# Kernel optimization log

Measured on AMD Instinct MI355X. Metric: run time of the kernel, lower is better.

## Reference

```python
import jax, jax.numpy as jnp
import numpy as np

N_NODES = 4096
IN_FEAT = 256
N_HEADS = 8
N_HIDDEN = 64  # out_features // n_heads
NEG_SLOPE = 0.2
EDGE_PROB = 0.05


def setup_inputs() -> dict:
    key = jax.random.key(0)
    k1, k2, k3, k4 = jax.random.split(key, 4)
    h = jax.random.normal(k1, (N_NODES, IN_FEAT), dtype=jnp.float32)
    # binary adjacency mask [N, N, 1] (broadcast over heads), as in the torch asserts
    adj_mat = (jax.random.uniform(k2, (N_NODES, N_NODES, 1)) < EDGE_PROB).astype(jnp.float32)
    # nn.Linear(in_features, n_heads*n_hidden, bias=False) weight: [H*F, in]
    W = jax.random.normal(k3, (N_HEADS * N_HIDDEN, IN_FEAT), dtype=jnp.float32) / np.sqrt(IN_FEAT)
    # nn.Linear(2*n_hidden, 1, bias=False) weight, flattened: [2*F]
    a = jax.random.normal(k4, (2 * N_HIDDEN,), dtype=jnp.float32) / np.sqrt(2 * N_HIDDEN)
    return {"h": h, "adj_mat": adj_mat, "W": W, "a": a}


def reference(h, adj_mat, W, a):
    n = h.shape[0]
    # g: [N, H, F]
    g = (h @ W.T).reshape(n, N_HEADS, N_HIDDEN)
    # attn(cat[g_i, g_j]) == a_l . g_i + a_r . g_j  (linear, no bias)
    a_l = a[:N_HIDDEN]
    a_r = a[N_HIDDEN:]
    el = jnp.einsum('ihf,f->ih', g, a_l)  # [N, H]
    er = jnp.einsum('jhf,f->jh', g, a_r)  # [N, H]
    e = jax.nn.leaky_relu(el[:, None, :] + er[None, :, :], NEG_SLOPE)  # [N, N, H]
    # note: original multiplies scores by adjacency (not masked_fill)
    e = e * adj_mat  # adj broadcasts over heads
    att = jax.nn.softmax(e, axis=1)  # softmax over source nodes j
    # dropout is identity at eval (dropout_rate=0.0)
    out = jnp.einsum('ijh,jhf->ihf', att, g)  # [N, H, F]
    return out.reshape(n, N_HEADS * N_HIDDEN)
```

## Files before the change

### kernel.cpp

```cpp
#include <hip/hip_runtime.h>

#define N_NODES 4096
#define IN_FEAT 256
#define N_HEADS 8
#define N_HIDDEN 64
#define OUT_FEAT (N_HEADS * N_HIDDEN)
#define NEG_SLOPE 0.2f

typedef _Float16 half8 __attribute__((ext_vector_type(8)));
typedef _Float16 h2 __attribute__((ext_vector_type(2)));
typedef float floatx4 __attribute__((ext_vector_type(4)));

__global__ __launch_bounds__(256) void produce(
    const float* __restrict__ H, const float* __restrict__ adj,
    const float* __restrict__ Wt, const float* __restrict__ a,
    _Float16* __restrict__ GT16, float* __restrict__ elT,
    _Float16* __restrict__ eR1h, _Float16* __restrict__ eR2h,
    unsigned long long* __restrict__ bits) {
  __shared__ _Float16 SM[4 * 64 * 64];
  const int t = threadIdx.x;
  const int bx = blockIdx.x, by = blockIdx.y;

  if (by >= 8) {
    const int c = bx * 8 + (by - 8);
    const size_t W0 = (size_t)c * 512;
    const int wv = t >> 6, lane = t & 63;
    for (int k0 = 0; k0 < 128; k0 += 8) {
      float v[8];
#pragma unroll
      for (int k = 0; k < 8; ++k)
        v[k] = adj[(W0 + wv * 128 + k0 + k) * 64 + lane];
#pragma unroll
      for (int k = 0; k < 8; ++k) {
        unsigned long long m = __ballot(v[k] != 0.f);
        if (lane == 0) bits[W0 + wv * 128 + k0 + k] = m;
      }
    }
    return;
  }

  _Float16* Ah = SM;
  _Float16* Al = SM + 4096;
  _Float16* Bh = SM + 8192;
  _Float16* Bl = SM + 12288;
  const int w = t >> 6, l = t & 63;
  const int n16 = l & 15, q = l >> 4;
  const int bi = bx, bo = by;
  const int m0 = bi * 64 + w * 16;

  floatx4 acc[4];
#pragma unroll
  for (int ct = 0; ct < 4; ++ct) acc[ct] = (floatx4)0.f;

  for (int kc = 0; kc < 4; ++kc) {
    if (kc) __syncthreads();
#pragma unroll
    for (int p = 0; p < 4; ++p) {
      const int idx = p * 256 + t;
      const int r = idx >> 4;
      const int c4 = (idx & 15) << 2;
      const int dst = r * 64 + ((((idx & 15) >> 1)) ^ (r & 7)) * 8 + (idx & 1) * 4;
      float4 hv = *(const float4*)(H + (size_t)(bi * 64 + r) * IN_FEAT + kc * 64 + c4);
      float4 wv = *(const float4*)(Wt + (size_t)(bo * 64 + r) * IN_FEAT + kc * 64 + c4);
      union { _Float16 h[4]; int2 d; } hh_, hl_, wh_, wl_;
      hh_.h[0] = (_Float16)hv.x; hh_.h[1] = (_Float16)hv.y;
      hh_.h[2] = (_Float16)hv.z; hh_.h[3] = (_Float16)hv.w;
      hl_.h[0] = (_Float16)(hv.x - (float)hh_.h[0]);
      hl_.h[1] = (_Float16)(hv.y - (float)hh_.h[1]);
      hl_.h[2] = (_Float16)(hv.z - (float)hh_.h[2]);
      hl_.h[3] = (_Float16)(hv.w - (float)hh_.h[3]);
      wh_.h[0] = (_Float16)wv.x; wh_.h[1] = (_Float16)wv.y;
      wh_.h[2] = (_Float16)wv.z; wh_.h[3] = (_Float16)wv.w;
      wl_.h[0] = (_Float16)(wv.x - (float)wh_.h[0]);
      wl_.h[1] = (_Float16)(wv.y - (float)wh_.h[1]);
      wl_.h[2] = (_Float16)(wv.z - (float)wh_.h[2]);
      wl_.h[3] = (_Float16)(wv.w - (float)wh_.h[3]);
      *(int2*)&Ah[dst] = hh_.d;
      *(int2*)&Al[dst] = hl_.d;
      *(int2*)&Bh[dst] = wh_.d;
      *(int2*)&Bl[dst] = wl_.d;
    }
    __syncthreads();
#pragma unroll
    for (int ks = 0; ks < 2; ++ks) {
      const int ao = (w * 16 + n16) * 64 + (((ks << 2) + q) ^ (n16 & 7)) * 8;
      half8 Afh = *(const half8*)&Ah[ao];
      half8 Afl = *(const half8*)&Al[ao];
#pragma unroll
      for (int ct = 0; ct < 4; ++ct) {
        const int bofs = (ct * 16 + n16) * 64 + (((ks << 2) + q) ^ (n16 & 7)) * 8;
        half8 Bfh = *(const half8*)&Bh[bofs];
        half8 Bfl = *(const half8*)&Bl[bofs];
        acc[ct] = __builtin_amdgcn_mfma_f32_16x16x32_f16(Afh, Bfh, acc[ct], 0, 0, 0);
        acc[ct] = __builtin_amdgcn_mfma_f32_16x16x32_f16(Afl, Bfh, acc[ct], 0, 0, 0);
        acc[ct] = __builtin_amdgcn_mfma_f32_16x16x32_f16(Afh, Bfl, acc[ct], 0, 0, 0);
      }
    }
  }

  float aLv[4], aRv[4];
#pragma unroll
  for (int ct = 0; ct < 4; ++ct) {
    aLv[ct] = a[ct * 16 + n16];
    aRv[ct] = a[64 + ct * 16 + n16];
  }
#pragma unroll
  for (int reg = 0; reg < 4; ++reg) {
    float sl = 0.f, sr = 0.f;
#pragma unroll
    for (int ct = 0; ct < 4; ++ct) {
      sl = fmaf(acc[ct][reg], aLv[ct], sl);
      sr = fmaf(acc[ct][reg], aRv[ct], sr);
    }
#pragma unroll
    for (int off = 1; off < 16; off <<= 1) {
      sl += __shfl_xor(sl, off);
      sr += __shfl_xor(sr, off);
    }
    if (n16 == 0) {
      const int rowi = m0 + q * 4 + reg;
      elT[(size_t)bo * N_NODES + rowi] = sl;
      eR1h[(size_t)bo * N_NODES + rowi] = (_Float16)__expf(sr);
      eR2h[(size_t)bo * N_NODES + rowi] = (_Float16)__expf(0.2f * sr);
    }
  }

  __syncthreads();
  _Float16* LG = SM;
#pragma unroll
  for (int ct = 0; ct < 4; ++ct)
#pragma unroll
    for (int reg = 0; reg < 4; ++reg)
      LG[(w * 16 + q * 4 + reg) * 72 + ct * 16 + n16] = (_Float16)acc[ct][reg];
  __syncthreads();
  {
    const int f = t >> 2, jq = t & 3;
    union { _Float16 hh[16]; int4 v[2]; } u;
#pragma unroll
    for (int k = 0; k < 16; ++k) u.hh[k] = LG[(jq * 16 + k) * 72 + f];
    _Float16* dst = GT16 + (size_t)(bo * 64 + f) * N_NODES + bi * 64 + jq * 16;
    *(int4*)dst = u.v[0];
    *(int4*)(dst + 8) = u.v[1];
  }
}

__global__ __launch_bounds__(256) void attn_v6(
    const unsigned long long* __restrict__ bits, const _Float16* __restrict__ GT16,
    const float* __restrict__ elT, const _Float16* __restrict__ eR1h,
    const _Float16* __restrict__ eR2h, float* __restrict__ out) {
  __shared__ __align__(16) _Float16 Gt[2][2][4096];
  __shared__ __align__(16) _Float16 eRs1[2][2][64];
  __shared__ __align__(16) _Float16 eRs2[2][2][64];
  __shared__ uint2 bitsS[2][2][32];
  __shared__ float eL1s[32], eL2s[32];
  __shared__ float Zh1[32], Zfull[32];

  const int t = threadIdx.x;
  const int ib = blockIdx.x, h = blockIdx.y;
  const int i0 = ib * 32;
  const int w = t >> 6, l = t & 63, n16 = l & 15, q = l >> 4;
  const int rt = w & 1, jh = w >> 1;

  const int gjh = t >> 7, sf = (t >> 1) & 63, hrow = t & 1;
  const _Float16* gsrc = GT16 + (size_t)(h * 64 + sf) * N_NODES + gjh * 2048 + hrow * 32;
  const int era = (t >> 3) & 1, erjh = t >> 4, erseg = t & 7;
  const int bro = (t - 32) & 31, brjh = (t - 32) >> 5;

  if (t < 32) {
    float e = elT[(size_t)h * N_NODES + i0 + t];
    eL1s[t] = __expf(e);
    eL2s[t] = __expf(0.2f * e);
  }
  {
#pragma unroll
    for (int g = 0; g < 4; ++g) {
      int4 v = *(const int4*)(gsrc + g * 8);
      *(int4*)&Gt[0][gjh][sf * 64 + ((hrow * 4 + g) ^ (sf & 7)) * 8] = v;
    }
    if (t < 32) {
      const _Float16* esrc = (era ? eR2h : eR1h) + (size_t)h * N_NODES + erjh * 2048 + erseg * 8;
      int4 v = *(const int4*)esrc;
      *(int4*)&(era ? eRs2 : eRs1)[0][erjh][erseg * 8] = v;
    } else if (t < 96) {
      bitsS[0][brjh][bro] = *(const uint2*)&bits[(size_t)(i0 + bro) * 64 + brjh * 32];
    }
  }
  __syncthreads();

  const _Float16 e1f = (_Float16)eL1s[rt * 16 + n16];
  const _Float16 e2f = (_Float16)eL2s[rt * 16 + n16];
  const h2 eL1h2 = {e1f, e1f};
  const h2 eL2h2 = {e2f, e2f};
  half8 Bones;
#pragma unroll
  for (int k = 0; k < 8; ++k) Bones[k] = (n16 == 0) ? (_Float16)1.f : (_Float16)0.f;

  floatx4 acc[4];
#pragma unroll
  for (int ft = 0; ft < 4; ++ft) acc[ft] = (floatx4)0.f;
  floatx4 acc5 = (floatx4)0.f;

  int par = 0;
  for (int step = 0; step < 32; ++step) {
    int4 gv[4]; int4 ev; uint2 bv2;
    const bool more = (step + 1 < 32);
    if (more) {
      const _Float16* gs = gsrc + (size_t)(step + 1) * 64;
#pragma unroll
      for (int g = 0; g < 4; ++g) gv[g] = *(const int4*)(gs + g * 8);
      if (t < 32) {
        const _Float16* esrc = (era ? eR2h : eR1h) + (size_t)h * N_NODES + erjh * 2048 +
                               (step + 1) * 64 + erseg * 8;
        ev = *(const int4*)esrc;
      } else if (t < 96) {
        bv2 = *(const uint2*)&bits[(size_t)(i0 + bro) * 64 + brjh * 32 + step + 1];
      }
    }
    const uint2 bw = bitsS[par][jh][rt * 16 + n16];
    const _Float16* gt = &Gt[par][jh][0];
#pragma unroll
    for (int ks = 0; ks < 2; ++ks) {
      const unsigned dw = ks ? bw.y : bw.x;
      const unsigned byte = (dw >> (q * 8)) & 0xffu;
      uint4 r1 = *(const uint4*)&eRs1[par][jh][ks * 32 + q * 8];
      uint4 r2 = *(const uint4*)&eRs2[par][jh][ks * 32 + q * 8];
      const unsigned r1a[4] = {r1.x, r1.y, r1.z, r1.w};
      const unsigned r2a[4] = {r2.x, r2.y, r2.z, r2.w};
      unsigned pr[4];
#pragma unroll
      for (int kk = 0; kk < 4; ++kk) {
        h2 pa = eL1h2 * __builtin_bit_cast(h2, r1a[kk]);
        h2 pb = eL2h2 * __builtin_bit_cast(h2, r2a[kk]);
        h2 pv = __builtin_elementwise_max(pa, pb);
        unsigned y = (byte >> (2 * kk)) & 3u;
        unsigned b01 = (y | (y << 15)) & 0x00010001u;
        unsigned keep = b01 * 0xffffu;
        pr[kk] = (__builtin_bit_cast(unsigned, pv) & keep) | (0x3C003C00u & ~keep);
      }
      const uint4 prv = {pr[0], pr[1], pr[2], pr[3]};
      half8 Af = __builtin_bit_cast(half8, prv);
#pragma unroll
      for (int ft = 0; ft < 4; ++ft) {
        half8 Bf = *(const half8*)&gt[(ft * 16 + n16) * 64 + (((ks << 2) + q) ^ (n16 & 7)) * 8];
        acc[ft] = __builtin_amdgcn_mfma_f32_16x16x32_f16(Af, Bf, acc[ft], 0, 0, 0);
      }
      acc5 = __builtin_amdgcn_mfma_f32_16x16x32_f16(Af, Bones, acc5, 0, 0, 0);
    }
    if (more) {
      const int np = par ^ 1;
#pragma unroll
      for (int g = 0; g < 4; ++g)
        *(int4*)&Gt[np][gjh][sf * 64 + ((hrow * 4 + g) ^ (sf & 7)) * 8] = gv[g];
      if (t < 32) {
        *(int4*)&(era ? eRs2 : eRs1)[np][erjh][erseg * 8] = ev;
      } else if (t < 96) {
        bitsS[np][brjh][bro] = bv2;
      }
    }
    __syncthreads();
    par ^= 1;
  }

  float* comb = (float*)&Gt[0][0][0];
  if (jh == 1) {
#pragma unroll
    for (int ft = 0; ft < 4; ++ft)
#pragma unroll
      for (int reg = 0; reg < 4; ++reg)
        comb[(rt * 16 + q * 4 + reg) * 68 + ft * 16 + n16] = acc[ft][reg];
    if (n16 == 0) {
#pragma unroll
      for (int reg = 0; reg < 4; ++reg) Zh1[rt * 16 + q * 4 + reg] = acc5[reg];
    }
  }
  __syncthreads();
  if (jh == 0) {
#pragma unroll
    for (int ft = 0; ft < 4; ++ft)
#pragma unroll
      for (int reg = 0; reg < 4; ++reg)
        acc[ft][reg] += comb[(rt * 16 + q * 4 + reg) * 68 + ft * 16 + n16];
    if (n16 == 0) {
#pragma unroll
      for (int reg = 0; reg < 4; ++reg) {
        const int row = rt * 16 + q * 4 + reg;
        Zfull[row] = acc5[reg] + Zh1[row];
      }
    }
  }
  __syncthreads();
  if (jh == 0) {
#pragma unroll
    for (int reg = 0; reg < 4; ++reg) {
      const int row = rt * 16 + q * 4 + reg;
      const float invz = 1.f / Zfull[row];
      float* op = out + (size_t)(i0 + row) * OUT_FEAT + h * 64;
#pragma unroll
      for (int ft = 0; ft < 4; ++ft) op[ft * 16 + n16] = acc[ft][reg] * invz;
    }
  }
}

extern "C" void kernel_launch(void* const* d_in, const int* in_sizes, int n_in,
                              void* d_out, int out_size, void* d_ws, size_t ws_size,
                              hipStream_t stream) {
  const float* h   = (const float*)d_in[0];
  const float* adj = (const float*)d_in[1];
  const float* W   = (const float*)d_in[2];
  const float* a   = (const float*)d_in[3];
  float* out = (float*)d_out;

  char* ws = (char*)d_ws;
  _Float16* GT16 = (_Float16*)ws;
  unsigned long long* bits = (unsigned long long*)(ws + 4u * 1024 * 1024);
  float* elT = (float*)(ws + 6u * 1024 * 1024);
  _Float16* eR1h = (_Float16*)(ws + 6u * 1024 * 1024 + 128 * 1024);
  _Float16* eR2h = (_Float16*)(ws + 6u * 1024 * 1024 + 192 * 1024);

  produce<<<dim3(64, 16), 256, 0, stream>>>(h, adj, W, a, GT16, elT, eR1h, eR2h, bits);
  attn_v6<<<dim3(128, 8), 256, 0, stream>>>(bits, GT16, elT, eR1h, eR2h, out);
}
```

Before: 160.6 us.

## Load MFMA operands directly from global into registers, dropping LDS staging

The attention kernel no longer stages G tiles, eR vectors and adjacency bits through double-buffered shared memory with a barrier every step. Each lane now loads its own MFMA B fragments, eR values and bitmask word straight from global memory into registers, prefetched one step ahead. The launch bound also requests 4 blocks per CU. This removes the LDS round-trip and per-step __syncthreads, but raises register pressure and relies on L1/L2 to absorb the duplicated global reads across waves and blocks.

Measured after the change: 258.7 us. +61.1%, slower.

```diff
diff --git a/kernel.cpp b/kernel.cpp
--- a/kernel.cpp
+++ b/kernel.cpp
@@ -144,14 +144,11 @@
   }
 }
 
-__global__ __launch_bounds__(256) void attn_v6(
+__global__ __launch_bounds__(256, 4) void attn_v7(
     const unsigned long long* __restrict__ bits, const _Float16* __restrict__ GT16,
     const float* __restrict__ elT, const _Float16* __restrict__ eR1h,
     const _Float16* __restrict__ eR2h, float* __restrict__ out) {
-  __shared__ __align__(16) _Float16 Gt[2][2][4096];
-  __shared__ __align__(16) _Float16 eRs1[2][2][64];
-  __shared__ __align__(16) _Float16 eRs2[2][2][64];
-  __shared__ uint2 bitsS[2][2][32];
+  __shared__ float comb[32 * 68];
   __shared__ float eL1s[32], eL2s[32];
   __shared__ float Zh1[32], Zfull[32];
 
@@ -161,29 +158,10 @@
   const int w = t >> 6, l = t & 63, n16 = l & 15, q = l >> 4;
   const int rt = w & 1, jh = w >> 1;
 
-  const int gjh = t >> 7, sf = (t >> 1) & 63, hrow = t & 1;
-  const _Float16* gsrc = GT16 + (size_t)(h * 64 + sf) * N_NODES + gjh * 2048 + hrow * 32;
-  const int era = (t >> 3) & 1, erjh = t >> 4, erseg = t & 7;
-  const int bro = (t - 32) & 31, brjh = (t - 32) >> 5;
-
   if (t < 32) {
     float e = elT[(size_t)h * N_NODES + i0 + t];
     eL1s[t] = __expf(e);
     eL2s[t] = __expf(0.2f * e);
-  }
-  {
-#pragma unroll
-    for (int g = 0; g < 4; ++g) {
-      int4 v = *(const int4*)(gsrc + g * 8);
-      *(int4*)&Gt[0][gjh][sf * 64 + ((hrow * 4 + g) ^ (sf & 7)) * 8] = v;
-    }
-    if (t < 32) {
-      const _Float16* esrc = (era ? eR2h : eR1h) + (size_t)h * N_NODES + erjh * 2048 + erseg * 8;
-      int4 v = *(const int4*)esrc;
-      *(int4*)&(era ? eRs2 : eRs1)[0][erjh][erseg * 8] = v;
-    } else if (t < 96) {
-      bitsS[0][brjh][bro] = *(const uint2*)&bits[(size_t)(i0 + bro) * 64 + brjh * 32];
-    }
   }
   __syncthreads();
 
@@ -195,37 +173,51 @@
 #pragma unroll
   for (int k = 0; k < 8; ++k) Bones[k] = (n16 == 0) ? (_Float16)1.f : (_Float16)0.f;
 
+  const _Float16* gb = GT16 + (size_t)(h * 64 + n16) * N_NODES + jh * 2048 + q * 8;
+  const _Float16* e1p = eR1h + (size_t)h * N_NODES + jh * 2048 + q * 8;
+  const _Float16* e2p = eR2h + (size_t)h * N_NODES + jh * 2048 + q * 8;
+  const unsigned long long* bp = bits + (size_t)(i0 + rt * 16 + n16) * 64 + jh * 32;
+
   floatx4 acc[4];
 #pragma unroll
   for (int ft = 0; ft < 4; ++ft) acc[ft] = (floatx4)0.f;
   floatx4 acc5 = (floatx4)0.f;
 
-  int par = 0;
+  half8 Bc[2][4];
+  uint4 r1c[2], r2c[2];
+  unsigned long long bvc;
+#pragma unroll
+  for (int ks = 0; ks < 2; ++ks) {
+#pragma unroll
+    for (int ft = 0; ft < 4; ++ft)
+      Bc[ks][ft] = *(const half8*)(gb + (size_t)ft * (16 * N_NODES) + ks * 32);
+    r1c[ks] = *(const uint4*)(e1p + ks * 32);
+    r2c[ks] = *(const uint4*)(e2p + ks * 32);
+  }
+  bvc = bp[0];
+
   for (int step = 0; step < 32; ++step) {
-    int4 gv[4]; int4 ev; uint2 bv2;
-    const bool more = (step + 1 < 32);
-    if (more) {
-      const _Float16* gs = gsrc + (size_t)(step + 1) * 64;
-#pragma unroll
-      for (int g = 0; g < 4; ++g) gv[g] = *(const int4*)(gs + g * 8);
-      if (t < 32) {
-        const _Float16* esrc = (era ? eR2h : eR1h) + (size_t)h * N_NODES + erjh * 2048 +
-                               (step + 1) * 64 + erseg * 8;
-        ev = *(const int4*)esrc;
-      } else if (t < 96) {
-        bv2 = *(const uint2*)&bits[(size_t)(i0 + bro) * 64 + brjh * 32 + step + 1];
-      }
-    }
-    const uint2 bw = bitsS[par][jh][rt * 16 + n16];
-    const _Float16* gt = &Gt[par][jh][0];
+    half8 Bn[2][4];
+    uint4 r1n[2], r2n[2];
+    unsigned long long bvn = bvc;
+    if (step + 1 < 32) {
+      const _Float16* gs = gb + (step + 1) * 64;
+#pragma unroll
+      for (int ks = 0; ks < 2; ++ks) {
+#pragma unroll
+        for (int ft = 0; ft < 4; ++ft)
+          Bn[ks][ft] = *(const half8*)(gs + (size_t)ft * (16 * N_NODES) + ks * 32);
+        r1n[ks] = *(const uint4*)(e1p + (step + 1) * 64 + ks * 32);
+        r2n[ks] = *(const uint4*)(e2p + (step + 1) * 64 + ks * 32);
+      }
+      bvn = bp[step + 1];
+    }
 #pragma unroll
     for (int ks = 0; ks < 2; ++ks) {
-      const unsigned dw = ks ? bw.y : bw.x;
+      const unsigned dw = (unsigned)(bvc >> (ks * 32));
       const unsigned byte = (dw >> (q * 8)) & 0xffu;
-      uint4 r1 = *(const uint4*)&eRs1[par][jh][ks * 32 + q * 8];
-      uint4 r2 = *(const uint4*)&eRs2[par][jh][ks * 32 + q * 8];
-      const unsigned r1a[4] = {r1.x, r1.y, r1.z, r1.w};
-      const unsigned r2a[4] = {r2.x, r2.y, r2.z, r2.w};
+      const unsigned r1a[4] = {r1c[ks].x, r1c[ks].y, r1c[ks].z, r1c[ks].w};
+      const unsigned r2a[4] = {r2c[ks].x, r2c[ks].y, r2c[ks].z, r2c[ks].w};
       unsigned pr[4];
 #pragma unroll
       for (int kk = 0; kk < 4; ++kk) {
@@ -240,28 +232,20 @@
       const uint4 prv = {pr[0], pr[1], pr[2], pr[3]};
       half8 Af = __builtin_bit_cast(half8, prv);
 #pragma unroll
-      for (int ft = 0; ft < 4; ++ft) {
-        half8 Bf = *(const half8*)&gt[(ft * 16 + n16) * 64 + (((ks << 2) + q) ^ (n16 & 7)) * 8];
-        acc[ft] = __builtin_amdgcn_mfma_f32_16x16x32_f16(Af, Bf, acc[ft], 0, 0, 0);
-      }
+      for (int ft = 0; ft < 4; ++ft)
+        acc[ft] = __builtin_amdgcn_mfma_f32_16x16x32_f16(Af, Bc[ks][ft], acc[ft], 0, 0, 0);
       acc5 = __builtin_amdgcn_mfma_f32_16x16x32_f16(Af, Bones, acc5, 0, 0, 0);
     }
-    if (more) {
-      const int np = par ^ 1;
-#pragma unroll
-      for (int g = 0; g < 4; ++g)
-        *(int4*)&Gt[np][gjh][sf * 64 + ((hrow * 4 + g) ^ (sf & 7)) * 8] = gv[g];
-      if (t < 32) {
-        *(int4*)&(era ? eRs2 : eRs1)[np][erjh][erseg * 8] = ev;
-      } else if (t < 96) {
-        bitsS[np][brjh][bro] = bv2;
-      }
-    }
-    __syncthreads();
-    par ^= 1;
-  }
-
-  float* comb = (float*)&Gt[0][0][0];
+#pragma unroll
+    for (int ks = 0; ks < 2; ++ks) {
+#pragma unroll
+      for (int ft = 0; ft < 4; ++ft) Bc[ks][ft] = Bn[ks][ft];
+      r1c[ks] = r1n[ks];
+      r2c[ks] = r2n[ks];
+    }
+    bvc = bvn;
+  }
+
   if (jh == 1) {
 #pragma unroll
     for (int ft = 0; ft < 4; ++ft)
@@ -318,5 +302,5 @@
   _Float16* eR2h = (_Float16*)(ws + 6u * 1024 * 1024 + 192 * 1024);
 
   produce<<<dim3(64, 16), 256, 0, stream>>>(h, adj, W, a, GT16, elT, eR1h, eR2h, bits);
-  attn_v6<<<dim3(128, 8), 256, 0, stream>>>(bits, GT16, elT, eR1h, eR2h, out);
+  attn_v7<<<dim3(128, 8), 256, 0, stream>>>(bits, GT16, elT, eR1h, eR2h, out);
 }
```

## Stream G tiles straight into LDS via global_load_lds and keep adjacency bits in registers

Applied to the files above, without the earlier changes.

The attention kernel now copies the G tile into shared memory with direct global-to-LDS loads (global_load_lds, 16 bytes per lane). It does this instead of loading into registers and writing back after the MFMA work, and the swizzle moves to the source addresses. Each thread also loads its own adjacency bitmask word straight into a register, one step ahead, so the shared-memory bits buffer goes away. This is meant to cut VGPR pressure and the LDS write instructions in the double-buffered loop. It relies on the barrier to order the async LDS writes, and if the vmcnt wait is not placed correctly the double buffer could race.

Result: faster. 156.1 us (-2.8%).

```diff
diff --git a/kernel.cpp b/kernel.cpp
--- a/kernel.cpp
+++ b/kernel.cpp
@@ -144,14 +144,13 @@
   }
 }
 
-__global__ __launch_bounds__(256) void attn_v6(
+__global__ __launch_bounds__(256) void attn_v8(
     const unsigned long long* __restrict__ bits, const _Float16* __restrict__ GT16,
     const float* __restrict__ elT, const _Float16* __restrict__ eR1h,
     const _Float16* __restrict__ eR2h, float* __restrict__ out) {
   __shared__ __align__(16) _Float16 Gt[2][2][4096];
   __shared__ __align__(16) _Float16 eRs1[2][2][64];
   __shared__ __align__(16) _Float16 eRs2[2][2][64];
-  __shared__ uint2 bitsS[2][2][32];
   __shared__ float eL1s[32], eL2s[32];
   __shared__ float Zh1[32], Zfull[32];
 
@@ -161,30 +160,38 @@
   const int w = t >> 6, l = t & 63, n16 = l & 15, q = l >> 4;
   const int rt = w & 1, jh = w >> 1;
 
-  const int gjh = t >> 7, sf = (t >> 1) & 63, hrow = t & 1;
-  const _Float16* gsrc = GT16 + (size_t)(h * 64 + sf) * N_NODES + gjh * 2048 + hrow * 32;
+  const _Float16* gsrcs[4];
+  int ldsbase[4];
+#pragma unroll
+  for (int c = 0; c < 4; ++c) {
+    const int flat = w * 256 + c * 64 + l;
+    const int fjh = flat >> 9;
+    const int ff = (flat >> 3) & 63;
+    const int ss = flat & 7;
+    const int cg = ss ^ (ff & 7);
+    gsrcs[c] = GT16 + (size_t)(h * 64 + ff) * N_NODES + fjh * 2048 + cg * 8;
+    ldsbase[c] = (w * 256 + c * 64) * 8;
+  }
   const int era = (t >> 3) & 1, erjh = t >> 4, erseg = t & 7;
-  const int bro = (t - 32) & 31, brjh = (t - 32) >> 5;
+  const _Float16* esrc0 = (era ? eR2h : eR1h) + (size_t)h * N_NODES + erjh * 2048 + erseg * 8;
+  const unsigned long long* bp = bits + (size_t)(i0 + rt * 16 + n16) * 64 + jh * 32;
 
   if (t < 32) {
     float e = elT[(size_t)h * N_NODES + i0 + t];
     eL1s[t] = __expf(e);
     eL2s[t] = __expf(0.2f * e);
   }
-  {
-#pragma unroll
-    for (int g = 0; g < 4; ++g) {
-      int4 v = *(const int4*)(gsrc + g * 8);
-      *(int4*)&Gt[0][gjh][sf * 64 + ((hrow * 4 + g) ^ (sf & 7)) * 8] = v;
-    }
-    if (t < 32) {
-      const _Float16* esrc = (era ? eR2h : eR1h) + (size_t)h * N_NODES + erjh * 2048 + erseg * 8;
-      int4 v = *(const int4*)esrc;
-      *(int4*)&(era ? eRs2 : eRs1)[0][erjh][erseg * 8] = v;
-    } else if (t < 96) {
-      bitsS[0][brjh][bro] = *(const uint2*)&bits[(size_t)(i0 + bro) * 64 + brjh * 32];
-    }
-  }
+#pragma unroll
+  for (int c = 0; c < 4; ++c)
+    __builtin_amdgcn_global_load_lds(
+        (const __attribute__((address_space(1))) unsigned int*)gsrcs[c],
+        (__attribute__((address_space(3))) unsigned int*)(&Gt[0][0][0] + ldsbase[c]),
+        16, 0, 0);
+  if (t < 32) {
+    int4 ev = *(const int4*)esrc0;
+    *(int4*)&(era ? eRs2 : eRs1)[0][erjh][erseg * 8] = ev;
+  }
+  unsigned long long bvc = bp[0];
   __syncthreads();
 
   const _Float16 e1f = (_Float16)eL1s[rt * 16 + n16];
@@ -202,25 +209,23 @@
 
   int par = 0;
   for (int step = 0; step < 32; ++step) {
-    int4 gv[4]; int4 ev; uint2 bv2;
-    const bool more = (step + 1 < 32);
-    if (more) {
-      const _Float16* gs = gsrc + (size_t)(step + 1) * 64;
-#pragma unroll
-      for (int g = 0; g < 4; ++g) gv[g] = *(const int4*)(gs + g * 8);
-      if (t < 32) {
-        const _Float16* esrc = (era ? eR2h : eR1h) + (size_t)h * N_NODES + erjh * 2048 +
-                               (step + 1) * 64 + erseg * 8;
-        ev = *(const int4*)esrc;
-      } else if (t < 96) {
-        bv2 = *(const uint2*)&bits[(size_t)(i0 + bro) * 64 + brjh * 32 + step + 1];
-      }
-    }
-    const uint2 bw = bitsS[par][jh][rt * 16 + n16];
+    int4 ev;
+    unsigned long long bvn = bvc;
+    if (step + 1 < 32) {
+      const int np = par ^ 1;
+#pragma unroll
+      for (int c = 0; c < 4; ++c)
+        __builtin_amdgcn_global_load_lds(
+            (const __attribute__((address_space(1))) unsigned int*)(gsrcs[c] + (step + 1) * 64),
+            (__attribute__((address_space(3))) unsigned int*)(&Gt[np][0][0] + ldsbase[c]),
+            16, 0, 0);
+      if (t < 32) ev = *(const int4*)(esrc0 + (step + 1) * 64);
+      bvn = bp[step + 1];
+    }
     const _Float16* gt = &Gt[par][jh][0];
 #pragma unroll
     for (int ks = 0; ks < 2; ++ks) {
-      const unsigned dw = ks ? bw.y : bw.x;
+      const unsigned dw = (unsigned)(bvc >> (ks * 32));
       const unsigned byte = (dw >> (q * 8)) & 0xffu;
       uint4 r1 = *(const uint4*)&eRs1[par][jh][ks * 32 + q * 8];
       uint4 r2 = *(const uint4*)&eRs2[par][jh][ks * 32 + q * 8];
@@ -246,17 +251,9 @@
       }
       acc5 = __builtin_amdgcn_mfma_f32_16x16x32_f16(Af, Bones, acc5, 0, 0, 0);
     }
-    if (more) {
-      const int np = par ^ 1;
-#pragma unroll
-      for (int g = 0; g < 4; ++g)
-        *(int4*)&Gt[np][gjh][sf * 64 + ((hrow * 4 + g) ^ (sf & 7)) * 8] = gv[g];
-      if (t < 32) {
-        *(int4*)&(era ? eRs2 : eRs1)[np][erjh][erseg * 8] = ev;
-      } else if (t < 96) {
-        bitsS[np][brjh][bro] = bv2;
-      }
-    }
+    if (step + 1 < 32 && t < 32)
+      *(int4*)&(era ? eRs2 : eRs1)[par ^ 1][erjh][erseg * 8] = ev;
+    bvc = bvn;
     __syncthreads();
     par ^= 1;
   }
@@ -318,5 +315,5 @@
   _Float16* eR2h = (_Float16*)(ws + 6u * 1024 * 1024 + 192 * 1024);
 
   produce<<<dim3(64, 16), 256, 0, stream>>>(h, adj, W, a, GT16, elT, eR1h, eR2h, bits);
-  attn_v6<<<dim3(128, 8), 256, 0, stream>>>(bits, GT16, elT, eR1h, eR2h, out);
+  attn_v8<<<dim3(128, 8), 256, 0, stream>>>(bits, GT16, elT, eR1h, eR2h, out);
 }
```
